# Performance work log

Measured on AMD Instinct MI355X. Metric: run time of the kernel, lower is better.

The kernel has to match this reference:

```python
import jax, jax.numpy as jnp
import numpy as np
import math

N, M, DIM = 16384, 4096, 1024


def setup_inputs() -> dict:
    key = jax.random.key(0)
    k1, k2, k3, k4, k5 = jax.random.split(key, 5)
    x = jax.random.normal(k1, (N, DIM), dtype=jnp.float32)
    e_repr = jax.random.normal(k2, (M, DIM), dtype=jnp.float32)
    H = jax.random.randint(k3, (N, M), 0, 2, dtype=jnp.int32)  # incidence matrix, >0 = connected
    # nn.Linear(dim, dim, bias=False) weights, scaled like torch default init
    W_e = jax.random.normal(k4, (DIM, DIM), dtype=jnp.float32) / math.sqrt(DIM)
    W_n = jax.random.normal(k5, (DIM, DIM), dtype=jnp.float32) / math.sqrt(DIM)
    return {"x": x, "e_repr": e_repr, "H": H, "W_e": W_e, "W_n": W_n}


def reference(x, e_repr, H, W_e, W_n):
    he = e_repr @ W_e.T            # [M, dim]  (W_e(e_repr); original recomputes this, same math)
    hn = x @ W_n.T                 # [N, dim]
    scale = 1.0 / math.sqrt(he.shape[1])
    B = (hn @ he.T) * scale        # [N, M] scores
    mask = H > 0
    B = jnp.where(mask, B, -1e9)
    B = jax.nn.softmax(B, axis=1) * mask.astype(B.dtype)
    out = jax.nn.elu(B @ he)       # [N, dim]
    return out, B
```

## Files before the change

### kernel.cpp

```cpp
#include <hip/hip_runtime.h>

#define NN 16384
#define MM 4096
#define DD 1024

typedef unsigned short u16;
typedef unsigned int u32;
typedef short bf16x8 __attribute__((ext_vector_type(8)));
typedef float f32x4 __attribute__((ext_vector_type(4)));

enum { EPI_MASK = 1, EPI_ELU = 2 };

__global__ void sentinel_kernel(float* out, float val) {
    if (blockIdx.x == 0 && threadIdx.x < 64) out[threadIdx.x] = val;
}

__device__ __forceinline__ void gload16(const void* g, void* l) {
    __builtin_amdgcn_global_load_lds(
        (const __attribute__((address_space(1))) void*)g,
        (__attribute__((address_space(3))) void*)l, 16, 0, 0);
}

__device__ __forceinline__ void split2(float f, u16& hi, u16& lo) {
    const u32 u = __float_as_uint(f);
    hi = (u16)(u >> 16);
    const float r = f - __uint_as_float(u & 0xffff0000u);
    lo = (u16)(__float_as_uint(r) >> 16);
}

__device__ __forceinline__ u16 f2bf_rtne(float f) {
    const u32 u = __float_as_uint(f);
    return (u16)((u + 0x7FFFu + ((u >> 16) & 1u)) >> 16);
}

__global__ __launch_bounds__(256) void gemm_f32_to_split(
    const float* __restrict__ A, const float* __restrict__ Bt,
    u16* __restrict__ Ch, u16* __restrict__ Cl, int Cc, int K)
{
    __shared__ u16 sAh[128][40];
    __shared__ u16 sAl[128][40];
    __shared__ u16 sBh[128][40];
    __shared__ u16 sBl[128][40];

    const int tid = threadIdx.x;
    const int lane = tid & 63;
    const int w = tid >> 6;
    const int wm = (w >> 1) * 64;
    const int wn = (w & 1) * 64;
    const int l15 = lane & 15;
    const int l4 = lane >> 4;
    const int rowBlk = blockIdx.y * 128;
    const int colBlk = blockIdx.x * 128;
    const int sr = tid >> 1;
    const int sk = (tid & 1) * 16;

    f32x4 acc[4][4] = {};
    union V16 { u16 u[16]; bf16x8 v[2]; };

    for (int k0 = 0; k0 < K; k0 += 32) {
        const float* pa = A + (size_t)(rowBlk + sr) * K + k0 + sk;
        const float* pb = Bt + (size_t)(colBlk + sr) * K + k0 + sk;

        V16 ah, al, bh, bl;
#pragma unroll
        for (int i = 0; i < 4; ++i) {
            const float4 va = *(const float4*)(pa + 4 * i);
            const float4 vb = *(const float4*)(pb + 4 * i);
            const float fa[4] = { va.x, va.y, va.z, va.w };
            const float fb[4] = { vb.x, vb.y, vb.z, vb.w };
#pragma unroll
            for (int j = 0; j < 4; ++j) {
                split2(fa[j], ah.u[4 * i + j], al.u[4 * i + j]);
                split2(fb[j], bh.u[4 * i + j], bl.u[4 * i + j]);
            }
        }

        __syncthreads();
        *(bf16x8*)&sAh[sr][sk]     = ah.v[0];
        *(bf16x8*)&sAh[sr][sk + 8] = ah.v[1];
        *(bf16x8*)&sAl[sr][sk]     = al.v[0];
        *(bf16x8*)&sAl[sr][sk + 8] = al.v[1];
        *(bf16x8*)&sBh[sr][sk]     = bh.v[0];
        *(bf16x8*)&sBh[sr][sk + 8] = bh.v[1];
        *(bf16x8*)&sBl[sr][sk]     = bl.v[0];
        *(bf16x8*)&sBl[sr][sk + 8] = bl.v[1];
        __syncthreads();

        bf16x8 a_h[4], a_l[4], b_h[4], b_l[4];
#pragma unroll
        for (int m = 0; m < 4; ++m) {
            const int r = wm + m * 16 + l15;
            a_h[m] = *(const bf16x8*)&sAh[r][l4 * 8];
            a_l[m] = *(const bf16x8*)&sAl[r][l4 * 8];
        }
#pragma unroll
        for (int n = 0; n < 4; ++n) {
            const int c = wn + n * 16 + l15;
            b_h[n] = *(const bf16x8*)&sBh[c][l4 * 8];
            b_l[n] = *(const bf16x8*)&sBl[c][l4 * 8];
        }

#pragma unroll
        for (int m = 0; m < 4; ++m)
#pragma unroll
            for (int n = 0; n < 4; ++n)
                acc[m][n] = __builtin_amdgcn_mfma_f32_16x16x32_bf16(a_h[m], b_h[n], acc[m][n], 0, 0, 0);
#pragma unroll
        for (int m = 0; m < 4; ++m)
#pragma unroll
            for (int n = 0; n < 4; ++n)
                acc[m][n] = __builtin_amdgcn_mfma_f32_16x16x32_bf16(a_h[m], b_l[n], acc[m][n], 0, 0, 0);
#pragma unroll
        for (int m = 0; m < 4; ++m)
#pragma unroll
            for (int n = 0; n < 4; ++n)
                acc[m][n] = __builtin_amdgcn_mfma_f32_16x16x32_bf16(a_l[m], b_h[n], acc[m][n], 0, 0, 0);
    }

    const size_t ldc = (size_t)Cc;
#pragma unroll
    for (int m = 0; m < 4; ++m) {
#pragma unroll
        for (int n = 0; n < 4; ++n) {
            const int col = colBlk + wn + n * 16 + l15;
#pragma unroll
            for (int r = 0; r < 4; ++r) {
                const int row = rowBlk + wm + m * 16 + l4 * 4 + r;
                u16 hi, lo;
                split2(acc[m][n][r], hi, lo);
                Ch[(size_t)row * ldc + col] = hi;
                if (Cl) Cl[(size_t)row * ldc + col] = lo;
            }
        }
    }
}

__global__ __launch_bounds__(256) void gemm_split_mask(
    const u16* __restrict__ Ah, const u16* __restrict__ Al,
    const u16* __restrict__ Bh, const u16* __restrict__ Bl,
    float* __restrict__ C, const int* __restrict__ Hm, int Cc, int K)
{
    __shared__ u16 sAh[128][32];
    __shared__ u16 sAl[128][32];
    __shared__ u16 sBh[128][32];
    __shared__ u16 sBl[128][32];

    const int tid = threadIdx.x;
    const int lane = tid & 63;
    const int w = tid >> 6;
    const int wm = (w >> 1) * 64;
    const int wn = (w & 1) * 64;
    const int l15 = lane & 15;
    const int l4 = lane >> 4;
    const int rowBlk = blockIdx.y * 128;
    const int colBlk = blockIdx.x * 128;

    const int srow = w * 32 + (lane >> 2);
    const int scol = ((lane & 3) ^ ((lane >> 3) & 3)) * 8;
    const int rchunk = (l4 ^ ((l15 >> 1) & 3)) * 8;

    f32x4 acc[4][4] = {};

    for (int k0 = 0; k0 < K; k0 += 32) {
        __syncthreads();
        const size_t ra = (size_t)(rowBlk + srow) * K + k0 + scol;
        const size_t rb = (size_t)(colBlk + srow) * K + k0 + scol;
        gload16(Ah + ra,                  &sAh[w * 32][0]);
        gload16(Ah + ra + (size_t)16 * K, &sAh[w * 32 + 16][0]);
        gload16(Al + ra,                  &sAl[w * 32][0]);
        gload16(Al + ra + (size_t)16 * K, &sAl[w * 32 + 16][0]);
        gload16(Bh + rb,                  &sBh[w * 32][0]);
        gload16(Bh + rb + (size_t)16 * K, &sBh[w * 32 + 16][0]);
        gload16(Bl + rb,                  &sBl[w * 32][0]);
        gload16(Bl + rb + (size_t)16 * K, &sBl[w * 32 + 16][0]);
        __syncthreads();

        bf16x8 a_h[4], a_l[4], b_h[4], b_l[4];
#pragma unroll
        for (int m = 0; m < 4; ++m) {
            const int r = wm + m * 16 + l15;
            a_h[m] = *(const bf16x8*)&sAh[r][rchunk];
            a_l[m] = *(const bf16x8*)&sAl[r][rchunk];
        }
#pragma unroll
        for (int n = 0; n < 4; ++n) {
            const int c = wn + n * 16 + l15;
            b_h[n] = *(const bf16x8*)&sBh[c][rchunk];
            b_l[n] = *(const bf16x8*)&sBl[c][rchunk];
        }

#pragma unroll
        for (int m = 0; m < 4; ++m)
#pragma unroll
            for (int n = 0; n < 4; ++n)
                acc[m][n] = __builtin_amdgcn_mfma_f32_16x16x32_bf16(a_h[m], b_h[n], acc[m][n], 0, 0, 0);
#pragma unroll
        for (int m = 0; m < 4; ++m)
#pragma unroll
            for (int n = 0; n < 4; ++n)
                acc[m][n] = __builtin_amdgcn_mfma_f32_16x16x32_bf16(a_h[m], b_l[n], acc[m][n], 0, 0, 0);
#pragma unroll
        for (int m = 0; m < 4; ++m)
#pragma unroll
            for (int n = 0; n < 4; ++n)
                acc[m][n] = __builtin_amdgcn_mfma_f32_16x16x32_bf16(a_l[m], b_h[n], acc[m][n], 0, 0, 0);
    }

    const size_t ldc = (size_t)Cc;
#pragma unroll
    for (int m = 0; m < 4; ++m) {
#pragma unroll
        for (int n = 0; n < 4; ++n) {
            const int col = colBlk + wn + n * 16 + l15;
#pragma unroll
            for (int r = 0; r < 4; ++r) {
                const int row = rowBlk + wm + m * 16 + l4 * 4 + r;
                float v = acc[m][n][r] * 0.03125f;
                if (Hm[(size_t)row * ldc + col] <= 0) v = -1e9f;
                C[(size_t)row * ldc + col] = v;
            }
        }
    }
}

__global__ __launch_bounds__(256) void gemm_bf16_elu(
    const u16* __restrict__ A, const u16* __restrict__ Bt,
    float* __restrict__ C, int Cc, int K)
{
    __shared__ u16 sA[128][32];
    __shared__ u16 sB[128][32];

    const int tid = threadIdx.x;
    const int lane = tid & 63;
    const int w = tid >> 6;
    const int wm = (w >> 1) * 64;
    const int wn = (w & 1) * 64;
    const int l15 = lane & 15;
    const int l4 = lane >> 4;
    const int rowBlk = blockIdx.y * 128;
    const int colBlk = blockIdx.x * 128;

    const int srow = w * 32 + (lane >> 2);
    const int scol = ((lane & 3) ^ ((lane >> 3) & 3)) * 8;
    const int rchunk = (l4 ^ ((l15 >> 1) & 3)) * 8;

    f32x4 acc[4][4] = {};

    for (int k0 = 0; k0 < K; k0 += 32) {
        __syncthreads();
        const size_t ra = (size_t)(rowBlk + srow) * K + k0 + scol;
        const size_t rb = (size_t)(colBlk + srow) * K + k0 + scol;
        gload16(A + ra,                   &sA[w * 32][0]);
        gload16(A + ra + (size_t)16 * K,  &sA[w * 32 + 16][0]);
        gload16(Bt + rb,                  &sB[w * 32][0]);
        gload16(Bt + rb + (size_t)16 * K, &sB[w * 32 + 16][0]);
        __syncthreads();

        bf16x8 a[4], b[4];
#pragma unroll
        for (int m = 0; m < 4; ++m)
            a[m] = *(const bf16x8*)&sA[wm + m * 16 + l15][rchunk];
#pragma unroll
        for (int n = 0; n < 4; ++n)
            b[n] = *(const bf16x8*)&sB[wn + n * 16 + l15][rchunk];

#pragma unroll
        for (int m = 0; m < 4; ++m)
#pragma unroll
            for (int n = 0; n < 4; ++n)
                acc[m][n] = __builtin_amdgcn_mfma_f32_16x16x32_bf16(a[m], b[n], acc[m][n], 0, 0, 0);
    }

    const size_t ldc = (size_t)Cc;
#pragma unroll
    for (int m = 0; m < 4; ++m) {
#pragma unroll
        for (int n = 0; n < 4; ++n) {
            const int col = colBlk + wn + n * 16 + l15;
#pragma unroll
            for (int r = 0; r < 4; ++r) {
                const int row = rowBlk + wm + m * 16 + l4 * 4 + r;
                float v = acc[m][n][r];
                v = v > 0.f ? v : (expf(v) - 1.f);
                C[(size_t)row * ldc + col] = v;
            }
        }
    }
}

__global__ __launch_bounds__(256) void softmax_rows_f32(
    float* __restrict__ Bm, u16* __restrict__ B16)
{
    const int row = blockIdx.x;
    const int tid = threadIdx.x;
    const int lane = tid & 63;
    const int wid = tid >> 6;
    float4* rp = reinterpret_cast<float4*>(Bm + (size_t)row * MM);

    float4 q[4];
#pragma unroll
    for (int i = 0; i < 4; ++i) q[i] = rp[i * 256 + tid];
    float v[16];
#pragma unroll
    for (int i = 0; i < 4; ++i) {
        v[4 * i + 0] = q[i].x; v[4 * i + 1] = q[i].y;
        v[4 * i + 2] = q[i].z; v[4 * i + 3] = q[i].w;
    }

    float mx = -3e38f;
#pragma unroll
    for (int i = 0; i < 16; ++i) mx = fmaxf(mx, v[i]);
#pragma unroll
    for (int off = 32; off >= 1; off >>= 1) mx = fmaxf(mx, __shfl_xor(mx, off));
    __shared__ float red[4];
    if (lane == 0) red[wid] = mx;
    __syncthreads();
    mx = fmaxf(fmaxf(red[0], red[1]), fmaxf(red[2], red[3]));
    __syncthreads();

    float e[16];
    float s = 0.f;
#pragma unroll
    for (int i = 0; i < 16; ++i) { e[i] = expf(v[i] - mx); s += e[i]; }
#pragma unroll
    for (int off = 32; off >= 1; off >>= 1) s += __shfl_xor(s, off);
    if (lane == 0) red[wid] = s;
    __syncthreads();
    s = red[0] + red[1] + red[2] + red[3];
    const float inv = (mx > -1e8f && s > 0.f) ? (1.0f / s) : 0.f;

    ushort4* hp = reinterpret_cast<ushort4*>(B16 + (size_t)row * MM);
#pragma unroll
    for (int i = 0; i < 4; ++i) {
        q[i].x = e[4 * i + 0] * inv; q[i].y = e[4 * i + 1] * inv;
        q[i].z = e[4 * i + 2] * inv; q[i].w = e[4 * i + 3] * inv;
        rp[i * 256 + tid] = q[i];
        ushort4 h;
        h.x = f2bf_rtne(q[i].x); h.y = f2bf_rtne(q[i].y);
        h.z = f2bf_rtne(q[i].z); h.w = f2bf_rtne(q[i].w);
        hp[i * 256 + tid] = h;
    }
}

extern "C" void kernel_launch(void* const* d_in, const int* in_sizes, int n_in,
                              void* d_out, int out_size, void* d_ws, size_t ws_size,
                              hipStream_t stream)
{
    (void)d_ws; (void)ws_size;

    float* O = (float*)d_out;
    bool ok_sizes = (n_in == 5)
        && in_sizes[0] == NN * DD && in_sizes[1] == MM * DD
        && in_sizes[2] == NN * MM
        && in_sizes[3] == DD * DD && in_sizes[4] == DD * DD;
    if (!ok_sizes) { sentinel_kernel<<<1, 64, 0, stream>>>(O, 1e6f); return; }
    if (out_size != NN * DD + NN * MM) { sentinel_kernel<<<1, 64, 0, stream>>>(O, 2e6f); return; }

    const float* x  = (const float*)d_in[0];
    const float* er = (const float*)d_in[1];
    const int*   Hm = (const int*)d_in[2];
    const float* We = (const float*)d_in[3];
    const float* Wn = (const float*)d_in[4];

    float* Bo = O + (size_t)NN * DD;

    u16* hn_h  = (u16*)O;
    u16* hn_l  = hn_h + (size_t)NN * DD;
    u16* he_h  = (u16*)d_in[0];
    u16* he_l  = he_h + (size_t)MM * DD;
    u16* heT_h = he_l + (size_t)MM * DD;
    u16* B16   = (u16*)d_in[2];

    dim3 blk(256);
    gemm_f32_to_split<<<dim3(DD / 128, NN / 128), blk, 0, stream>>>(x, Wn, hn_h, hn_l, DD, DD);
    gemm_f32_to_split<<<dim3(DD / 128, MM / 128), blk, 0, stream>>>(er, We, he_h, he_l, DD, DD);
    gemm_f32_to_split<<<dim3(MM / 128, DD / 128), blk, 0, stream>>>(We, er, heT_h, nullptr, MM, DD);
    gemm_split_mask<<<dim3(MM / 128, NN / 128), blk, 0, stream>>>(
        hn_h, hn_l, he_h, he_l, Bo, Hm, MM, DD);
    softmax_rows_f32<<<dim3(NN), blk, 0, stream>>>(Bo, B16);
    gemm_bf16_elu<<<dim3(DD / 128, NN / 128), blk, 0, stream>>>(B16, heT_h, O, DD, MM);
}
```

Baseline: 1.453 ms.

## Pre-split fp32 inputs to bf16 and double-buffer LDS in all GEMMs

Adds a standalone split pass that converts x, e_repr, W_e and W_n into bf16 hi/lo arrays once, staged in the B output region as scratch. The projection GEMMs then use the same async global-to-LDS loading path as the score GEMM instead of splitting fp32 tiles in registers. All GEMMs (templated gemm_ps3 and gemm_bf16_elu) gain double-buffered shared memory, so the next k-tile is prefetched while MFMAs run and one barrier per iteration is removed. The cost is extra memory traffic for the split pass and doubled LDS use per block, which may lower occupancy.

```diff
diff --git a/kernel.cpp b/kernel.cpp
--- a/kernel.cpp
+++ b/kernel.cpp
@@ -9,7 +9,7 @@
 typedef short bf16x8 __attribute__((ext_vector_type(8)));
 typedef float f32x4 __attribute__((ext_vector_type(4)));
 
-enum { EPI_MASK = 1, EPI_ELU = 2 };
+enum { EPI_SPLIT = 0, EPI_SPLITH = 1, EPI_MASK = 2 };
 
 __global__ void sentinel_kernel(float* out, float val) {
     if (blockIdx.x == 0 && threadIdx.x < 64) out[threadIdx.x] = val;
@@ -33,14 +33,34 @@
     return (u16)((u + 0x7FFFu + ((u >> 16) & 1u)) >> 16);
 }
 
-__global__ __launch_bounds__(256) void gemm_f32_to_split(
-    const float* __restrict__ A, const float* __restrict__ Bt,
-    u16* __restrict__ Ch, u16* __restrict__ Cl, int Cc, int K)
-{
-    __shared__ u16 sAh[128][40];
-    __shared__ u16 sAl[128][40];
-    __shared__ u16 sBh[128][40];
-    __shared__ u16 sBl[128][40];
+__global__ __launch_bounds__(256) void split_f32(
+    const float* __restrict__ src, u16* __restrict__ hi, u16* __restrict__ lo,
+    long n4)
+{
+    long i = (long)blockIdx.x * 256 + threadIdx.x;
+    const long stride = (long)gridDim.x * 256;
+    for (; i < n4; i += stride) {
+        const float4 v = ((const float4*)src)[i];
+        ushort4 h, l;
+        split2(v.x, h.x, l.x); split2(v.y, h.y, l.y);
+        split2(v.z, h.z, l.z); split2(v.w, h.w, l.w);
+        ((ushort4*)hi)[i] = h;
+        ((ushort4*)lo)[i] = l;
+    }
+}
+
+template <int EPI>
+__global__ __launch_bounds__(256) void gemm_ps3(
+    const u16* __restrict__ Ah, const u16* __restrict__ Al,
+    const u16* __restrict__ Bh, const u16* __restrict__ Bl,
+    u16* __restrict__ Ch, u16* __restrict__ Cl,
+    float* __restrict__ Cf, const int* __restrict__ Hm,
+    int Cc, int K)
+{
+    __shared__ u16 sAh[2][128][32];
+    __shared__ u16 sAl[2][128][32];
+    __shared__ u16 sBh[2][128][32];
+    __shared__ u16 sBl[2][128][32];
 
     const int tid = threadIdx.x;
     const int lane = tid & 63;
@@ -51,99 +71,98 @@
     const int l4 = lane >> 4;
     const int rowBlk = blockIdx.y * 128;
     const int colBlk = blockIdx.x * 128;
-    const int sr = tid >> 1;
-    const int sk = (tid & 1) * 16;
+
+    const int srow = w * 32 + (lane >> 2);
+    const int scol = ((lane & 3) ^ ((lane >> 3) & 3)) * 8;
+    const int rchunk = (l4 ^ ((l15 >> 1) & 3)) * 8;
 
     f32x4 acc[4][4] = {};
-    union V16 { u16 u[16]; bf16x8 v[2]; };
+
+    auto stage = [&](int b, int k0) {
+        const size_t ra = (size_t)(rowBlk + srow) * K + k0 + scol;
+        const size_t rb = (size_t)(colBlk + srow) * K + k0 + scol;
+        gload16(Ah + ra,                  &sAh[b][w * 32][0]);
+        gload16(Ah + ra + (size_t)16 * K, &sAh[b][w * 32 + 16][0]);
+        gload16(Al + ra,                  &sAl[b][w * 32][0]);
+        gload16(Al + ra + (size_t)16 * K, &sAl[b][w * 32 + 16][0]);
+        gload16(Bh + rb,                  &sBh[b][w * 32][0]);
+        gload16(Bh + rb + (size_t)16 * K, &sBh[b][w * 32 + 16][0]);
+        gload16(Bl + rb,                  &sBl[b][w * 32][0]);
+        gload16(Bl + rb + (size_t)16 * K, &sBl[b][w * 32 + 16][0]);
+    };
+
+    stage(0, 0);
+    __syncthreads();
+    int cur = 0;
 
     for (int k0 = 0; k0 < K; k0 += 32) {
-        const float* pa = A + (size_t)(rowBlk + sr) * K + k0 + sk;
-        const float* pb = Bt + (size_t)(colBlk + sr) * K + k0 + sk;
-
-        V16 ah, al, bh, bl;
-#pragma unroll
-        for (int i = 0; i < 4; ++i) {
-            const float4 va = *(const float4*)(pa + 4 * i);
-            const float4 vb = *(const float4*)(pb + 4 * i);
-            const float fa[4] = { va.x, va.y, va.z, va.w };
-            const float fb[4] = { vb.x, vb.y, vb.z, vb.w };
-#pragma unroll
-            for (int j = 0; j < 4; ++j) {
-                split2(fa[j], ah.u[4 * i + j], al.u[4 * i + j]);
-                split2(fb[j], bh.u[4 * i + j], bl.u[4 * i + j]);
+        if (k0 + 32 < K) stage(cur ^ 1, k0 + 32);
+
+        bf16x8 a_h[4], a_l[4], b_h[4], b_l[4];
+#pragma unroll
+        for (int m = 0; m < 4; ++m) {
+            const int r = wm + m * 16 + l15;
+            a_h[m] = *(const bf16x8*)&sAh[cur][r][rchunk];
+            a_l[m] = *(const bf16x8*)&sAl[cur][r][rchunk];
+        }
+#pragma unroll
+        for (int n = 0; n < 4; ++n) {
+            const int c = wn + n * 16 + l15;
+            b_h[n] = *(const bf16x8*)&sBh[cur][c][rchunk];
+            b_l[n] = *(const bf16x8*)&sBl[cur][c][rchunk];
+        }
+
+#pragma unroll
+        for (int m = 0; m < 4; ++m)
+#pragma unroll
+            for (int n = 0; n < 4; ++n)
+                acc[m][n] = __builtin_amdgcn_mfma_f32_16x16x32_bf16(a_h[m], b_h[n], acc[m][n], 0, 0, 0);
+#pragma unroll
+        for (int m = 0; m < 4; ++m)
+#pragma unroll
+            for (int n = 0; n < 4; ++n)
+                acc[m][n] = __builtin_amdgcn_mfma_f32_16x16x32_bf16(a_h[m], b_l[n], acc[m][n], 0, 0, 0);
+#pragma unroll
+        for (int m = 0; m < 4; ++m)
+#pragma unroll
+            for (int n = 0; n < 4; ++n)
+                acc[m][n] = __builtin_amdgcn_mfma_f32_16x16x32_bf16(a_l[m], b_h[n], acc[m][n], 0, 0, 0);
+
+        __syncthreads();
+        cur ^= 1;
+    }
+
+    const size_t ldc = (size_t)Cc;
+#pragma unroll
+    for (int m = 0; m < 4; ++m) {
+#pragma unroll
+        for (int n = 0; n < 4; ++n) {
+            const int col = colBlk + wn + n * 16 + l15;
+#pragma unroll
+            for (int r = 0; r < 4; ++r) {
+                const int row = rowBlk + wm + m * 16 + l4 * 4 + r;
+                const size_t idx = (size_t)row * ldc + col;
+                if constexpr (EPI == EPI_MASK) {
+                    float v = acc[m][n][r] * 0.03125f;
+                    if (Hm[idx] <= 0) v = -1e9f;
+                    Cf[idx] = v;
+                } else {
+                    u16 hi, lo;
+                    split2(acc[m][n][r], hi, lo);
+                    Ch[idx] = hi;
+                    if constexpr (EPI == EPI_SPLIT) Cl[idx] = lo;
+                }
             }
         }
-
-        __syncthreads();
-        *(bf16x8*)&sAh[sr][sk]     = ah.v[0];
-        *(bf16x8*)&sAh[sr][sk + 8] = ah.v[1];
-        *(bf16x8*)&sAl[sr][sk]     = al.v[0];
-        *(bf16x8*)&sAl[sr][sk + 8] = al.v[1];
-        *(bf16x8*)&sBh[sr][sk]     = bh.v[0];
-        *(bf16x8*)&sBh[sr][sk + 8] = bh.v[1];
-        *(bf16x8*)&sBl[sr][sk]     = bl.v[0];
-        *(bf16x8*)&sBl[sr][sk + 8] = bl.v[1];
-        __syncthreads();
-
-        bf16x8 a_h[4], a_l[4], b_h[4], b_l[4];
-#pragma unroll
-        for (int m = 0; m < 4; ++m) {
-            const int r = wm + m * 16 + l15;
-            a_h[m] = *(const bf16x8*)&sAh[r][l4 * 8];
-            a_l[m] = *(const bf16x8*)&sAl[r][l4 * 8];
-        }
-#pragma unroll
-        for (int n = 0; n < 4; ++n) {
-            const int c = wn + n * 16 + l15;
-            b_h[n] = *(const bf16x8*)&sBh[c][l4 * 8];
-            b_l[n] = *(const bf16x8*)&sBl[c][l4 * 8];
-        }
-
-#pragma unroll
-        for (int m = 0; m < 4; ++m)
-#pragma unroll
-            for (int n = 0; n < 4; ++n)
-                acc[m][n] = __builtin_amdgcn_mfma_f32_16x16x32_bf16(a_h[m], b_h[n], acc[m][n], 0, 0, 0);
-#pragma unroll
-        for (int m = 0; m < 4; ++m)
-#pragma unroll
-            for (int n = 0; n < 4; ++n)
-                acc[m][n] = __builtin_amdgcn_mfma_f32_16x16x32_bf16(a_h[m], b_l[n], acc[m][n], 0, 0, 0);
-#pragma unroll
-        for (int m = 0; m < 4; ++m)
-#pragma unroll
-            for (int n = 0; n < 4; ++n)
-                acc[m][n] = __builtin_amdgcn_mfma_f32_16x16x32_bf16(a_l[m], b_h[n], acc[m][n], 0, 0, 0);
-    }
-
-    const size_t ldc = (size_t)Cc;
-#pragma unroll
-    for (int m = 0; m < 4; ++m) {
-#pragma unroll
-        for (int n = 0; n < 4; ++n) {
-            const int col = colBlk + wn + n * 16 + l15;
-#pragma unroll
-            for (int r = 0; r < 4; ++r) {
-                const int row = rowBlk + wm + m * 16 + l4 * 4 + r;
-                u16 hi, lo;
-                split2(acc[m][n][r], hi, lo);
-                Ch[(size_t)row * ldc + col] = hi;
-                if (Cl) Cl[(size_t)row * ldc + col] = lo;
-            }
-        }
-    }
-}
-
-__global__ __launch_bounds__(256) void gemm_split_mask(
-    const u16* __restrict__ Ah, const u16* __restrict__ Al,
-    const u16* __restrict__ Bh, const u16* __restrict__ Bl,
-    float* __restrict__ C, const int* __restrict__ Hm, int Cc, int K)
-{
-    __shared__ u16 sAh[128][32];
-    __shared__ u16 sAl[128][32];
-    __shared__ u16 sBh[128][32];
-    __shared__ u16 sBl[128][32];
+    }
+}
+
+__global__ __launch_bounds__(256) void gemm_bf16_elu(
+    const u16* __restrict__ A, const u16* __restrict__ Bt,
+    float* __restrict__ C, int Cc, int K)
+{
+    __shared__ u16 sA[2][128][32];
+    __shared__ u16 sB[2][128][32];
 
     const int tid = threadIdx.x;
     const int lane = tid & 63;
@@ -161,114 +180,38 @@
 
     f32x4 acc[4][4] = {};
 
-    for (int k0 = 0; k0 < K; k0 += 32) {
-        __syncthreads();
+    auto stage = [&](int b, int k0) {
         const size_t ra = (size_t)(rowBlk + srow) * K + k0 + scol;
         const size_t rb = (size_t)(colBlk + srow) * K + k0 + scol;
-        gload16(Ah + ra,                  &sAh[w * 32][0]);
-        gload16(Ah + ra + (size_t)16 * K, &sAh[w * 32 + 16][0]);
-        gload16(Al + ra,                  &sAl[w * 32][0]);
-        gload16(Al + ra + (size_t)16 * K, &sAl[w * 32 + 16][0]);
-        gload16(Bh + rb,                  &sBh[w * 32][0]);
-        gload16(Bh + rb + (size_t)16 * K, &sBh[w * 32 + 16][0]);
-        gload16(Bl + rb,                  &sBl[w * 32][0]);
-        gload16(Bl + rb + (size_t)16 * K, &sBl[w * 32 + 16][0]);
-        __syncthreads();
-
-        bf16x8 a_h[4], a_l[4], b_h[4], b_l[4];
-#pragma unroll
-        for (int m = 0; m < 4; ++m) {
-            const int r = wm + m * 16 + l15;
-            a_h[m] = *(const bf16x8*)&sAh[r][rchunk];
-            a_l[m] = *(const bf16x8*)&sAl[r][rchunk];
-        }
-#pragma unroll
-        for (int n = 0; n < 4; ++n) {
-            const int c = wn + n * 16 + l15;
-            b_h[n] = *(const bf16x8*)&sBh[c][rchunk];
-            b_l[n] = *(const bf16x8*)&sBl[c][rchunk];
-        }
-
-#pragma unroll
-        for (int m = 0; m < 4; ++m)
-#pragma unroll
-            for (int n = 0; n < 4; ++n)
-                acc[m][n] = __builtin_amdgcn_mfma_f32_16x16x32_bf16(a_h[m], b_h[n], acc[m][n], 0, 0, 0);
-#pragma unroll
-        for (int m = 0; m < 4; ++m)
-#pragma unroll
-            for (int n = 0; n < 4; ++n)
-                acc[m][n] = __builtin_amdgcn_mfma_f32_16x16x32_bf16(a_h[m], b_l[n], acc[m][n], 0, 0, 0);
-#pragma unroll
-        for (int m = 0; m < 4; ++m)
-#pragma unroll
-            for (int n = 0; n < 4; ++n)
-                acc[m][n] = __builtin_amdgcn_mfma_f32_16x16x32_bf16(a_l[m], b_h[n], acc[m][n], 0, 0, 0);
-    }
-
-    const size_t ldc = (size_t)Cc;
-#pragma unroll
-    for (int m = 0; m < 4; ++m) {
-#pragma unroll
-        for (int n = 0; n < 4; ++n) {
-            const int col = colBlk + wn + n * 16 + l15;
-#pragma unroll
-            for (int r = 0; r < 4; ++r) {
-                const int row = rowBlk + wm + m * 16 + l4 * 4 + r;
-                float v = acc[m][n][r] * 0.03125f;
-                if (Hm[(size_t)row * ldc + col] <= 0) v = -1e9f;
-                C[(size_t)row * ldc + col] = v;
-            }
-        }
-    }
-}
-
-__global__ __launch_bounds__(256) void gemm_bf16_elu(
-    const u16* __restrict__ A, const u16* __restrict__ Bt,
-    float* __restrict__ C, int Cc, int K)
-{
-    __shared__ u16 sA[128][32];
-    __shared__ u16 sB[128][32];
-
-    const int tid = threadIdx.x;
-    const int lane = tid & 63;
-    const int w = tid >> 6;
-    const int wm = (w >> 1) * 64;
-    const int wn = (w & 1) * 64;
-    const int l15 = lane & 15;
-    const int l4 = lane >> 4;
-    const int rowBlk = blockIdx.y * 128;
-    const int colBlk = blockIdx.x * 128;
-
-    const int srow = w * 32 + (lane >> 2);
-    const int scol = ((lane & 3) ^ ((lane >> 3) & 3)) * 8;
-    const int rchunk = (l4 ^ ((l15 >> 1) & 3)) * 8;
-
-    f32x4 acc[4][4] = {};
+        gload16(A + ra,                   &sA[b][w * 32][0]);
+        gload16(A + ra + (size_t)16 * K,  &sA[b][w * 32 + 16][0]);
+        gload16(Bt + rb,                  &sB[b][w * 32][0]);
+        gload16(Bt + rb + (size_t)16 * K, &sB[b][w * 32 + 16][0]);
+    };
+
+    stage(0, 0);
+    __syncthreads();
+    int cur = 0;
 
     for (int k0 = 0; k0 < K; k0 += 32) {
-        __syncthreads();
-        const size_t ra = (size_t)(rowBlk + srow) * K + k0 + scol;
-        const size_t rb = (size_t)(colBlk + srow) * K + k0 + scol;
-        gload16(A + ra,                   &sA[w * 32][0]);
-        gload16(A + ra + (size_t)16 * K,  &sA[w * 32 + 16][0]);
-        gload16(Bt + rb,                  &sB[w * 32][0]);
-        gload16(Bt + rb + (size_t)16 * K, &sB[w * 32 + 16][0]);
-        __syncthreads();
+        if (k0 + 32 < K) stage(cur ^ 1, k0 + 32);
 
         bf16x8 a[4], b[4];
 #pragma unroll
         for (int m = 0; m < 4; ++m)
-            a[m] = *(const bf16x8*)&sA[wm + m * 16 + l15][rchunk];
+            a[m] = *(const bf16x8*)&sA[cur][wm + m * 16 + l15][rchunk];
 #pragma unroll
         for (int n = 0; n < 4; ++n)
-            b[n] = *(const bf16x8*)&sB[wn + n * 16 + l15][rchunk];
+            b[n] = *(const bf16x8*)&sB[cur][wn + n * 16 + l15][rchunk];
 
 #pragma unroll
         for (int m = 0; m < 4; ++m)
 #pragma unroll
             for (int n = 0; n < 4; ++n)
                 acc[m][n] = __builtin_amdgcn_mfma_f32_16x16x32_bf16(a[m], b[n], acc[m][n], 0, 0, 0);
+
+        __syncthreads();
+        cur ^= 1;
     }
 
     const size_t ldc = (size_t)Cc;
@@ -364,6 +307,15 @@
 
     float* Bo = O + (size_t)NN * DD;
 
+    u16* xs_h  = (u16*)Bo;
+    u16* xs_l  = xs_h  + (size_t)NN * DD;
+    u16* ers_h = xs_l  + (size_t)NN * DD;
+    u16* ers_l = ers_h + (size_t)MM * DD;
+    u16* wes_h = ers_l + (size_t)MM * DD;
+    u16* wes_l = wes_h + (size_t)DD * DD;
+    u16* wns_h = wes_l + (size_t)DD * DD;
+    u16* wns_l = wns_h + (size_t)DD * DD;
+
     u16* hn_h  = (u16*)O;
     u16* hn_l  = hn_h + (size_t)NN * DD;
     u16* he_h  = (u16*)d_in[0];
@@ -372,11 +324,18 @@
     u16* B16   = (u16*)d_in[2];
 
     dim3 blk(256);
-    gemm_f32_to_split<<<dim3(DD / 128, NN / 128), blk, 0, stream>>>(x, Wn, hn_h, hn_l, DD, DD);
-    gemm_f32_to_split<<<dim3(DD / 128, MM / 128), blk, 0, stream>>>(er, We, he_h, he_l, DD, DD);
-    gemm_f32_to_split<<<dim3(MM / 128, DD / 128), blk, 0, stream>>>(We, er, heT_h, nullptr, MM, DD);
-    gemm_split_mask<<<dim3(MM / 128, NN / 128), blk, 0, stream>>>(
-        hn_h, hn_l, he_h, he_l, Bo, Hm, MM, DD);
+    split_f32<<<dim3(2048), blk, 0, stream>>>(x,  xs_h,  xs_l,  (long)NN * DD / 4);
+    split_f32<<<dim3(1024), blk, 0, stream>>>(er, ers_h, ers_l, (long)MM * DD / 4);
+    split_f32<<<dim3(512),  blk, 0, stream>>>(We, wes_h, wes_l, (long)DD * DD / 4);
+    split_f32<<<dim3(512),  blk, 0, stream>>>(Wn, wns_h, wns_l, (long)DD * DD / 4);
+    gemm_ps3<EPI_SPLIT><<<dim3(DD / 128, NN / 128), blk, 0, stream>>>(
+        xs_h, xs_l, wns_h, wns_l, hn_h, hn_l, nullptr, nullptr, DD, DD);
+    gemm_ps3<EPI_SPLIT><<<dim3(DD / 128, MM / 128), blk, 0, stream>>>(
+        ers_h, ers_l, wes_h, wes_l, he_h, he_l, nullptr, nullptr, DD, DD);
+    gemm_ps3<EPI_SPLITH><<<dim3(MM / 128, DD / 128), blk, 0, stream>>>(
+        wes_h, wes_l, ers_h, ers_l, heT_h, nullptr, nullptr, nullptr, MM, DD);
+    gemm_ps3<EPI_MASK><<<dim3(MM / 128, NN / 128), blk, 0, stream>>>(
+        hn_h, hn_l, he_h, he_l, nullptr, nullptr, Bo, Hm, MM, DD);
     softmax_rows_f32<<<dim3(NN), blk, 0, stream>>>(Bo, B16);
     gemm_bf16_elu<<<dim3(DD / 128, NN / 128), blk, 0, stream>>>(B16, heT_h, O, DD, MM);
 }
```

New measurement: 1.431 ms. No clear change (-1.5%).
